# Kernel tuning notes

Measured on AMD Instinct MI355X. Metric: run time of the kernel, lower is better.

The kernel has to match this reference:

```python
import jax, jax.numpy as jnp
import numpy as np

SEQ_FEAT = 1024   # sequence_length (input feature dim of Linear layers)
ATT = 512         # attention_size
P_DROP = 0.2
B, T = 8, 2048


def setup_inputs() -> dict:
    key = jax.random.key(0)
    k1, k2, k3, k4, k5 = jax.random.split(key, 5)
    s = 1.0 / np.sqrt(SEQ_FEAT)
    x = jax.random.normal(k1, (B, T, SEQ_FEAT), dtype=jnp.float32)
    Wq = jax.random.normal(k2, (ATT, SEQ_FEAT), dtype=jnp.float32) * s
    Wk = jax.random.normal(k3, (ATT, SEQ_FEAT), dtype=jnp.float32) * s
    Wv = jax.random.normal(k4, (SEQ_FEAT, SEQ_FEAT), dtype=jnp.float32) * s
    drop_mask = jax.random.uniform(k5, (B, T, T)) >= P_DROP  # keep where True
    return {"x": x, "Wq": Wq, "Wk": Wk, "Wv": Wv, "drop_mask": drop_mask}


def reference(x, Wq, Wk, Wv, drop_mask):
    # Linear (no bias): y = x @ W.T, torch Linear weight is [out, in]
    q = jnp.einsum('btf,af->bta', x, Wq)          # [B,T,ATT]
    k = jnp.einsum('btf,af->bta', x, Wk)          # [B,T,ATT]
    v = jnp.einsum('btf,gf->btg', x, Wv)          # [B,T,SEQ_FEAT]
    scores = jnp.einsum('bta,bsa->bts', q, k) / jnp.sqrt(jnp.float32(ATT))
    attn = jax.nn.softmax(scores, axis=-1)
    # dropout (training=True in F.dropout): scale kept entries by 1/(1-p)
    attn = jnp.where(drop_mask, attn / (1.0 - P_DROP), 0.0)
    out = jnp.einsum('bts,bsg->btg', attn, v)     # [B,T,SEQ_FEAT]
    return out
```

## Files before the change

### kernel.cpp

```cpp
#include <hip/hip_runtime.h>

typedef unsigned short u16;
typedef _Float16 h16;
typedef __attribute__((ext_vector_type(4))) float f32x4;
typedef __attribute__((ext_vector_type(8))) _Float16 h16x8;
typedef __attribute__((ext_vector_type(4))) _Float16 h16x4;
typedef __attribute__((ext_vector_type(4))) int i32x4;

__global__ __launch_bounds__(256) void k_cast_all(
    const float* __restrict__ x, const float* __restrict__ wq,
    const float* __restrict__ wk, const float* __restrict__ wv,
    h16* __restrict__ xf, h16* __restrict__ wqk, h16* __restrict__ wvf) {
  int bid = blockIdx.x;
  const float* src;
  h16* dst;
  int idx;
  if (bid < 16384) { src = x;  dst = xf;           idx = bid * 256 + threadIdx.x; }
  else if (bid < 16896) { src = wq; dst = wqk;          idx = (bid - 16384) * 256 + threadIdx.x; }
  else if (bid < 17408) { src = wk; dst = wqk + 524288; idx = (bid - 16896) * 256 + threadIdx.x; }
  else { src = wv; dst = wvf;          idx = (bid - 17408) * 256 + threadIdx.x; }
  f32x4 v = ((const f32x4*)src)[idx];
  h16x4 o;
#pragma unroll
  for (int e = 0; e < 4; ++e) o[e] = (h16)v[e];
  ((h16x4*)dst)[idx] = o;
}

__device__ __forceinline__ void gl16(const u16* src, u16* dst) {
  __builtin_amdgcn_global_load_lds(
      (const __attribute__((address_space(1))) unsigned*)src,
      (__attribute__((address_space(3))) unsigned*)dst, 16, 0, 0);
}

__device__ __forceinline__ void swz_block(int& bn, int& bm, int& bz) {
  int gx = gridDim.x, gy = gridDim.y;
  int flat = blockIdx.x + gx * (blockIdx.y + gy * blockIdx.z);
  int nwg = gx * gy * (int)gridDim.z;
  int q = nwg >> 3;
  int id = (flat & 7) * q + (flat >> 3);
  bn = id % gx;
  id /= gx;
  bm = id % gy;
  bz = id / gy;
}

template <int NT, int EPI>
__global__ __launch_bounds__(512, 2) void k_gemm(
    const u16* __restrict__ A, int lda, long long aZ,
    const u16* __restrict__ B, int ldb, long long bZ,
    void* __restrict__ Cp, int ldc, long long cZ, float scale) {
  __shared__ u16 lds[2 * 32768];
  int bn, bm, bz;
  swz_block(bn, bm, bz);
  const int tid = threadIdx.x;
  const int lane = tid & 63, wid = tid >> 6;
  const int wr = wid >> 2, wc = wid & 3;
  const u16* A0 = A + (size_t)bz * aZ + (size_t)bm * 256 * lda;
  const u16* B0 = B + (size_t)bz * bZ + (size_t)bn * 256 * ldb;

  const int lc = ((tid & 3) ^ ((tid >> 3) & 3)) << 3;
  const int r0s = tid >> 2;

  auto STAGE = [&](int t, int op, int kh) {
    if (t >= NT) return;
    int kk = (t << 6) + (kh << 5);
    const u16* g = op ? B0 : A0;
    int ld_ = op ? ldb : lda;
    u16* dst = &lds[0] + (t & 1) * 32768 + op * 16384 + kh * 8192;
    gl16(g + (size_t)r0s * ld_ + kk + lc, dst + tid * 8);
    gl16(g + (size_t)(r0s + 128) * ld_ + kk + lc, dst + 4096 + tid * 8);
  };

  const int fr = lane & 15;
  const int pch = (((lane >> 4) ^ ((fr >> 1) & 3)) << 3);
  const int abase = (wr * 128 + fr) * 32 + pch;
  const int bbase = 16384 + (wc * 64 + fr) * 32 + pch;

  f32x4 acc[8][4] = {};

  STAGE(0, 0, 0); STAGE(0, 0, 1); STAGE(0, 1, 0); STAGE(0, 1, 1);
  STAGE(1, 1, 0); STAGE(1, 0, 0); STAGE(1, 1, 1);
  asm volatile("s_waitcnt vmcnt(6)" ::: "memory");
  __builtin_amdgcn_s_barrier();

  auto TILE = [&](int T, int c, bool drain) {
    const int cb = c * 32768;
    h16x8 av[4], bv[4];
#pragma unroll
    for (int n = 0; n < 4; ++n) bv[n] = *(const h16x8*)&lds[cb + bbase + n * 512];
#pragma unroll
    for (int m = 0; m < 4; ++m) av[m] = *(const h16x8*)&lds[cb + abase + m * 512];
    STAGE(T + 1, 0, 1);
    __builtin_amdgcn_s_barrier();
    asm volatile("s_waitcnt lgkmcnt(0)" ::: "memory");
    __builtin_amdgcn_s_setprio(1);
#pragma unroll
    for (int m = 0; m < 4; ++m)
#pragma unroll
      for (int n = 0; n < 4; ++n)
        acc[m][n] = __builtin_amdgcn_mfma_f32_16x16x32_f16(av[m], bv[n], acc[m][n], 0, 0, 0);
    __builtin_amdgcn_s_setprio(0);
    __builtin_amdgcn_s_barrier();
#pragma unroll
    for (int m = 0; m < 4; ++m) av[m] = *(const h16x8*)&lds[cb + abase + 2048 + m * 512];
    STAGE(T + 2, 1, 0);
    __builtin_amdgcn_s_barrier();
    asm volatile("s_waitcnt lgkmcnt(0)" ::: "memory");
    __builtin_amdgcn_s_setprio(1);
#pragma unroll
    for (int m = 0; m < 4; ++m)
#pragma unroll
      for (int n = 0; n < 4; ++n)
        acc[m + 4][n] = __builtin_amdgcn_mfma_f32_16x16x32_f16(av[m], bv[n], acc[m + 4][n], 0, 0, 0);
    __builtin_amdgcn_s_setprio(0);
    __builtin_amdgcn_s_barrier();
#pragma unroll
    for (int n = 0; n < 4; ++n) bv[n] = *(const h16x8*)&lds[cb + bbase + 8192 + n * 512];
#pragma unroll
    for (int m = 0; m < 4; ++m) av[m] = *(const h16x8*)&lds[cb + abase + 8192 + m * 512];
    STAGE(T + 2, 0, 0);
    __builtin_amdgcn_s_barrier();
    asm volatile("s_waitcnt lgkmcnt(0)" ::: "memory");
    __builtin_amdgcn_s_setprio(1);
#pragma unroll
    for (int m = 0; m < 4; ++m)
#pragma unroll
      for (int n = 0; n < 4; ++n)
        acc[m][n] = __builtin_amdgcn_mfma_f32_16x16x32_f16(av[m], bv[n], acc[m][n], 0, 0, 0);
    __builtin_amdgcn_s_setprio(0);
    __builtin_amdgcn_s_barrier();
#pragma unroll
    for (int m = 0; m < 4; ++m) av[m] = *(const h16x8*)&lds[cb + abase + 8192 + 2048 + m * 512];
    STAGE(T + 2, 1, 1);
    if (drain)
      asm volatile("s_waitcnt vmcnt(0)" ::: "memory");
    else
      asm volatile("s_waitcnt vmcnt(6)" ::: "memory");
    __builtin_amdgcn_s_barrier();
    asm volatile("s_waitcnt lgkmcnt(0)" ::: "memory");
    __builtin_amdgcn_s_setprio(1);
#pragma unroll
    for (int m = 0; m < 4; ++m)
#pragma unroll
      for (int n = 0; n < 4; ++n)
        acc[m + 4][n] = __builtin_amdgcn_mfma_f32_16x16x32_f16(av[m], bv[n], acc[m + 4][n], 0, 0, 0);
    __builtin_amdgcn_s_setprio(0);
    __builtin_amdgcn_s_barrier();
  };

#pragma unroll 1
  for (int T = 0; T < NT; T += 2) {
    TILE(T, 0, T == NT - 2);
    TILE(T + 1, 1, T + 1 == NT - 1);
  }

  const size_t zc = (size_t)bz * cZ;
#pragma unroll
  for (int m = 0; m < 8; ++m)
#pragma unroll
    for (int n = 0; n < 4; ++n)
#pragma unroll
      for (int r = 0; r < 4; ++r) {
        int row = bm * 256 + wr * 128 + m * 16 + (lane >> 4) * 4 + r;
        int col = bn * 256 + wc * 64 + n * 16 + fr;
        float f = acc[m][n][r];
        if constexpr (EPI == 0) {
          ((h16*)Cp)[zc + (size_t)row * ldc + col] = (h16)f;
        } else if constexpr (EPI == 1) {
          ((float*)Cp)[zc + (size_t)row * ldc + col] = f * scale;
        } else {
          ((h16*)Cp)[zc + (size_t)row * ldc + col] = (h16)(f * scale);
        }
      }
}

__global__ __launch_bounds__(256) void k_softmax(const h16* __restrict__ sc,
                                                 h16* __restrict__ P,
                                                 const int* __restrict__ mask) {
  const size_t rowp = blockIdx.x;
  const h16* srow = sc + rowp * 2048;
  h16* prow = P + rowp * 2048;
  const int* mrow = mask + rowp * 2048;
  const int tid = threadIdx.x;
  h16x8 hv = ((const h16x8*)srow)[tid];
  float v[8];
#pragma unroll
  for (int j = 0; j < 8; ++j) v[j] = (float)hv[j];
  float m = v[0];
#pragma unroll
  for (int j = 1; j < 8; ++j) m = fmaxf(m, v[j]);
#pragma unroll
  for (int o = 32; o >= 1; o >>= 1) m = fmaxf(m, __shfl_xor(m, o));
  __shared__ float redm[4], reds[4];
  if ((tid & 63) == 0) redm[tid >> 6] = m;
  __syncthreads();
  m = fmaxf(fmaxf(redm[0], redm[1]), fmaxf(redm[2], redm[3]));
  float e[8], s = 0.f;
#pragma unroll
  for (int j = 0; j < 8; ++j) { e[j] = __expf(v[j] - m); s += e[j]; }
#pragma unroll
  for (int o = 32; o >= 1; o >>= 1) s += __shfl_xor(s, o);
  if ((tid & 63) == 0) reds[tid >> 6] = s;
  __syncthreads();
  s = reds[0] + reds[1] + reds[2] + reds[3];
  const float inv = 1.0f / (0.8f * s);
  i32x4 m0 = ((const i32x4*)mrow)[tid * 2];
  i32x4 m1 = ((const i32x4*)mrow)[tid * 2 + 1];
  int mm[8] = {m0[0], m0[1], m0[2], m0[3], m1[0], m1[1], m1[2], m1[3]};
  h16x8 o;
#pragma unroll
  for (int j = 0; j < 8; ++j) o[j] = mm[j] ? (h16)(e[j] * inv) : (h16)0.f;
  ((h16x8*)prow)[tid] = o;
}

extern "C" void kernel_launch(void* const* d_in, const int* in_sizes, int n_in,
                              void* d_out, int out_size, void* d_ws, size_t ws_size,
                              hipStream_t stream) {
  const float* x  = (const float*)d_in[0];
  const float* Wq = (const float*)d_in[1];
  const float* Wk = (const float*)d_in[2];
  const float* Wv = (const float*)d_in[3];
  const int* mask = (const int*)d_in[4];
  float* out = (float*)d_out;

  u16* ws = (u16*)d_ws;
  h16* xf  = (h16*)ws;
  h16* Wqk = (h16*)(ws + 16777216);
  h16* Wvf = (h16*)(ws + 17825792);
  h16* qk  = (h16*)(ws + 18874368);
  h16* vvt = (h16*)(ws + 35651584);
  h16* Pb  = (h16*)(ws + 52428864);
  h16* sch = (h16*)(ws + 85983296);

  k_cast_all<<<18432, 256, 0, stream>>>(x, Wq, Wk, Wv, xf, Wqk, Wvf);

  dim3 gqk(4, 64, 1);
  k_gemm<16, 0><<<gqk, 512, 0, stream>>>((const u16*)xf, 1024, 0,
                                         (const u16*)Wqk, 1024, 0, qk, 1024, 0, 0.f);

  dim3 gvt(64, 4, 1);
  k_gemm<16, 0><<<gvt, 512, 0, stream>>>((const u16*)Wvf, 1024, 0,
                                         (const u16*)xf, 1024, 0, vvt, 16384, 0, 0.f);

  const float scale = 0.044194173824159216f;
  dim3 gs(8, 8, 8);
  k_gemm<8, 4><<<gs, 512, 0, stream>>>((const u16*)qk, 1024, 2097152,
                                       (const u16*)(qk + 512), 1024, 2097152,
                                       sch, 2048, 4194304, scale);

  k_softmax<<<16384, 256, 0, stream>>>(sch, Pb, mask);

  dim3 gpv(4, 8, 8);
  k_gemm<32, 1><<<gpv, 512, 0, stream>>>((const u16*)Pb, 2048, 4194304,
                                         (const u16*)vvt, 16384, 2048,
                                         out, 1024, 2097152, 1.0f);

  (void)in_sizes; (void)n_in; (void)out_size; (void)ws_size;
}
```

Before: 268.4 us.

## Simplify GEMM main loop to plain double-buffered prefetch with one barrier per tile

Replaces the finely interleaved four-phase tile schedule, which had staggered partial-tile prefetches and many barriers, with a simpler double buffer. Each iteration loads all A/B fragments for a k-half, issues the full next-tile prefetch, runs the MFMAs, and ends with a full vmcnt(0) wait and a single barrier. This removes most of the barrier and waitcnt overhead and doubles the A fragment registers (av[8]). In exchange, global loads only get one tile of compute to hide under, and the extra registers may lower occupancy.

```diff
diff --git a/kernel.cpp b/kernel.cpp
--- a/kernel.cpp
+++ b/kernel.cpp
@@ -79,79 +79,40 @@
   f32x4 acc[8][4] = {};
 
   STAGE(0, 0, 0); STAGE(0, 0, 1); STAGE(0, 1, 0); STAGE(0, 1, 1);
-  STAGE(1, 1, 0); STAGE(1, 0, 0); STAGE(1, 1, 1);
-  asm volatile("s_waitcnt vmcnt(6)" ::: "memory");
+  asm volatile("s_waitcnt vmcnt(0)" ::: "memory");
   __builtin_amdgcn_s_barrier();
-
-  auto TILE = [&](int T, int c, bool drain) {
-    const int cb = c * 32768;
-    h16x8 av[4], bv[4];
+  asm volatile("" ::: "memory");
+
+#pragma unroll 1
+  for (int T = 0; T < NT; ++T) {
+    const int cb = (T & 1) * 32768;
+    h16x8 av[8], bv[4];
 #pragma unroll
     for (int n = 0; n < 4; ++n) bv[n] = *(const h16x8*)&lds[cb + bbase + n * 512];
 #pragma unroll
-    for (int m = 0; m < 4; ++m) av[m] = *(const h16x8*)&lds[cb + abase + m * 512];
-    STAGE(T + 1, 0, 1);
-    __builtin_amdgcn_s_barrier();
-    asm volatile("s_waitcnt lgkmcnt(0)" ::: "memory");
+    for (int m = 0; m < 8; ++m) av[m] = *(const h16x8*)&lds[cb + abase + m * 512];
+    STAGE(T + 1, 0, 0); STAGE(T + 1, 0, 1); STAGE(T + 1, 1, 0); STAGE(T + 1, 1, 1);
     __builtin_amdgcn_s_setprio(1);
 #pragma unroll
-    for (int m = 0; m < 4; ++m)
+    for (int m = 0; m < 8; ++m)
 #pragma unroll
       for (int n = 0; n < 4; ++n)
         acc[m][n] = __builtin_amdgcn_mfma_f32_16x16x32_f16(av[m], bv[n], acc[m][n], 0, 0, 0);
     __builtin_amdgcn_s_setprio(0);
-    __builtin_amdgcn_s_barrier();
-#pragma unroll
-    for (int m = 0; m < 4; ++m) av[m] = *(const h16x8*)&lds[cb + abase + 2048 + m * 512];
-    STAGE(T + 2, 1, 0);
-    __builtin_amdgcn_s_barrier();
-    asm volatile("s_waitcnt lgkmcnt(0)" ::: "memory");
+#pragma unroll
+    for (int n = 0; n < 4; ++n) bv[n] = *(const h16x8*)&lds[cb + bbase + 8192 + n * 512];
+#pragma unroll
+    for (int m = 0; m < 8; ++m) av[m] = *(const h16x8*)&lds[cb + abase + 8192 + m * 512];
     __builtin_amdgcn_s_setprio(1);
 #pragma unroll
-    for (int m = 0; m < 4; ++m)
-#pragma unroll
-      for (int n = 0; n < 4; ++n)
-        acc[m + 4][n] = __builtin_amdgcn_mfma_f32_16x16x32_f16(av[m], bv[n], acc[m + 4][n], 0, 0, 0);
-    __builtin_amdgcn_s_setprio(0);
-    __builtin_amdgcn_s_barrier();
-#pragma unroll
-    for (int n = 0; n < 4; ++n) bv[n] = *(const h16x8*)&lds[cb + bbase + 8192 + n * 512];
-#pragma unroll
-    for (int m = 0; m < 4; ++m) av[m] = *(const h16x8*)&lds[cb + abase + 8192 + m * 512];
-    STAGE(T + 2, 0, 0);
-    __builtin_amdgcn_s_barrier();
-    asm volatile("s_waitcnt lgkmcnt(0)" ::: "memory");
-    __builtin_amdgcn_s_setprio(1);
-#pragma unroll
-    for (int m = 0; m < 4; ++m)
+    for (int m = 0; m < 8; ++m)
 #pragma unroll
       for (int n = 0; n < 4; ++n)
         acc[m][n] = __builtin_amdgcn_mfma_f32_16x16x32_f16(av[m], bv[n], acc[m][n], 0, 0, 0);
     __builtin_amdgcn_s_setprio(0);
+    asm volatile("s_waitcnt vmcnt(0)" ::: "memory");
     __builtin_amdgcn_s_barrier();
-#pragma unroll
-    for (int m = 0; m < 4; ++m) av[m] = *(const h16x8*)&lds[cb + abase + 8192 + 2048 + m * 512];
-    STAGE(T + 2, 1, 1);
-    if (drain)
-      asm volatile("s_waitcnt vmcnt(0)" ::: "memory");
-    else
-      asm volatile("s_waitcnt vmcnt(6)" ::: "memory");
-    __builtin_amdgcn_s_barrier();
-    asm volatile("s_waitcnt lgkmcnt(0)" ::: "memory");
-    __builtin_amdgcn_s_setprio(1);
-#pragma unroll
-    for (int m = 0; m < 4; ++m)
-#pragma unroll
-      for (int n = 0; n < 4; ++n)
-        acc[m + 4][n] = __builtin_amdgcn_mfma_f32_16x16x32_f16(av[m], bv[n], acc[m + 4][n], 0, 0, 0);
-    __builtin_amdgcn_s_setprio(0);
-    __builtin_amdgcn_s_barrier();
-  };
-
-#pragma unroll 1
-  for (int T = 0; T < NT; T += 2) {
-    TILE(T, 0, T == NT - 2);
-    TILE(T + 1, 1, T + 1 == NT - 1);
+    asm volatile("" ::: "memory");
   }
 
   const size_t zc = (size_t)bz * cZ;
```

Result: no change. 272.3 us (+1.4%).
